# Kernel tuning notes

Measured on AMD Instinct MI355X. Metric: run time of the kernel, lower is better.

Reference implementation:

```python
import jax, jax.numpy as jnp
import numpy as np

N, E = 10000, 30000
D_IN, E_DIM, H1, H2, C = 64, 16, 128, 64, 10


def setup_inputs() -> dict:
    key = jax.random.key(0)
    ks = jax.random.split(key, 12)
    x = jax.random.normal(ks[0], (N, D_IN), dtype=jnp.float32)
    edge_attr = jax.random.normal(ks[1], (E, E_DIM), dtype=jnp.float32)
    edge_index = jax.random.randint(ks[2], (2, E), 0, N, dtype=jnp.int64)
    # linear1: D_IN -> H1
    W1 = jax.random.normal(ks[3], (D_IN, H1), dtype=jnp.float32) / np.sqrt(D_IN)
    b1 = jnp.zeros((H1,), dtype=jnp.float32)
    # edge MLP 1: E_DIM -> H1*H2
    We1 = jax.random.normal(ks[4], (E_DIM, H1 * H2), dtype=jnp.float32) / np.sqrt(E_DIM)
    be1 = jnp.zeros((H1 * H2,), dtype=jnp.float32)
    root1 = jax.random.uniform(ks[5], (H1, H2), dtype=jnp.float32,
                               minval=-1.0 / np.sqrt(H1), maxval=1.0 / np.sqrt(H1))
    bias1 = jnp.zeros((H2,), dtype=jnp.float32)
    # edge MLP 2: E_DIM -> H2*C
    We2 = jax.random.normal(ks[6], (E_DIM, H2 * C), dtype=jnp.float32) / np.sqrt(E_DIM)
    be2 = jnp.zeros((H2 * C,), dtype=jnp.float32)
    root2 = jax.random.uniform(ks[7], (H2, C), dtype=jnp.float32,
                               minval=-1.0 / np.sqrt(H2), maxval=1.0 / np.sqrt(H2))
    bias2 = jnp.zeros((C,), dtype=jnp.float32)
    return {"x": x, "edge_attr": edge_attr, "edge_index": edge_index,
            "W1": W1, "b1": b1, "We1": We1, "be1": be1, "root1": root1, "bias1": bias1,
            "We2": We2, "be2": be2, "root2": root2, "bias2": bias2}


def _nnconv(h, src, dst, edge_attr, We, be, root, bias, c_in, c_out):
    # per-edge weight matrix from edge MLP: [E, c_in, c_out]
    W_e = (edge_attr @ We + be).reshape(-1, c_in, c_out)
    msg = jnp.einsum('ei,eio->eo', h[src], W_e)          # gather + batched matmul
    agg = jax.ops.segment_sum(msg, dst, num_segments=N)   # scatter-add to target nodes
    return agg + h @ root + bias


def reference(x, edge_attr, edge_index, W1, b1, We1, be1, root1, bias1,
              We2, be2, root2, bias2):
    src, dst = edge_index[0], edge_index[1]  # PyG: x_j = x[src], aggregate at dst
    h = jax.nn.relu(x @ W1 + b1)                               # [N, H1]
    h = jax.nn.relu(_nnconv(h, src, dst, edge_attr, We1, be1, root1, bias1, H1, H2))
    z = _nnconv(h, src, dst, edge_attr, We2, be2, root2, bias2, H2, C)
    return jax.nn.log_softmax(z, axis=1)
```

## Files before the change

### kernel.cpp

```cpp
#include <hip/hip_runtime.h>

#define N_NODES 10000
#define N_EDGES 30000
#define DIN     64
#define EDIM    16
#define H1      128
#define H2      64
#define C_OUT   10

typedef __bf16 bfrag __attribute__((ext_vector_type(8)));
typedef float  f32x4 __attribute__((ext_vector_type(4)));

__device__ __forceinline__ ushort f2bf(float f) {
    union { float f; unsigned u; } x; x.f = f;
    unsigned r = x.u + 0x7fffu + ((x.u >> 16) & 1u);
    return (ushort)(r >> 16);
}
__device__ __forceinline__ float bf2f(ushort s) {
    union { unsigned u; float f; } x; x.u = ((unsigned)s) << 16;
    return x.f;
}

#define KA_B1   1250
#define KA_B2   (KA_B1 + 576)
#define KA_B3   (KA_B2 + 48)
#define KA_B4   (KA_B3 + 181)
__global__ __launch_bounds__(256) void kA_prep(
        const float* __restrict__ x, const float* __restrict__ W1,
        const float* __restrict__ b1,
        const float* __restrict__ We1, const float* __restrict__ root1,
        const float* __restrict__ be1,
        const float* __restrict__ We2, const float* __restrict__ be2,
        const float* __restrict__ root2,
        ushort* __restrict__ h_bf, ushort* __restrict__ B1t,
        ushort* __restrict__ B2t, float* __restrict__ aggz) {
    int t = threadIdx.x;
    int bx = blockIdx.x;
    if (bx < KA_B1) {
        __shared__ float w_lds[DIN * H1];
        __shared__ float b_lds[H1];
        __shared__ float x_lds[8][DIN];
        for (int idx = t; idx < DIN * H1 / 4; idx += 256)
            ((float4*)w_lds)[idx] = ((const float4*)W1)[idx];
        if (t < H1) b_lds[t] = b1[t];
        int n0 = bx * 8;
        if (t < 128) {
            int row = t >> 4, c4 = t & 15;
            int n = n0 + row;
            float4 v = make_float4(0.f, 0.f, 0.f, 0.f);
            if (n < N_NODES) v = ((const float4*)(x + (size_t)n * DIN))[c4];
            ((float4*)(x_lds[row]))[c4] = v;
        }
        __syncthreads();
        int nl = t >> 5;
        int o  = (t & 31) * 4;
        int n  = n0 + nl;
        float4 acc = *(const float4*)&b_lds[o];
        #pragma unroll 8
        for (int i = 0; i < DIN; ++i) {
            float xv = x_lds[nl][i];
            float4 w = *(const float4*)&w_lds[i * H1 + o];
            acc.x = fmaf(xv, w.x, acc.x);
            acc.y = fmaf(xv, w.y, acc.y);
            acc.z = fmaf(xv, w.z, acc.z);
            acc.w = fmaf(xv, w.w, acc.w);
        }
        if (n < N_NODES) {
            ushort4 s;
            s.x = f2bf(fmaxf(acc.x, 0.f));
            s.y = f2bf(fmaxf(acc.y, 0.f));
            s.z = f2bf(fmaxf(acc.z, 0.f));
            s.w = f2bf(fmaxf(acc.w, 0.f));
            *(ushort4*)&h_bf[(size_t)n * H1 + o] = s;
        }
    } else if (bx < KA_B2) {
        int idx = (bx - KA_B1) * 256 + t;
        int c = idx >> 7, i = idx & 127;
        float v;
        if (c < 1024)      v = We1[(size_t)(c >> 6) * (H1 * H2) + i * 64 + (c & 63)];
        else if (c < 1088) v = root1[i * 64 + (c - 1024)];
        else               v = be1[i * 64 + (c - 1088)];
        B1t[idx] = f2bf(v);
    } else if (bx < KA_B3) {
        int idx = (bx - KA_B2) * 256 + t;
        int c = idx >> 6, j = idx & 63;
        float v = 0.f;
        if (c < 160)      v = We2[(size_t)(c / 10) * 640 + j * 10 + (c % 10)];
        else if (c < 170) v = be2[j * 10 + (c - 160)];
        else if (c < 180) v = root2[j * 10 + (c - 170)];
        B2t[idx] = f2bf(v);
    } else {
        int zb = bx - KA_B3;
        for (int i = zb * 256 + t; i < 185000; i += 181 * 256)
            ((float4*)aggz)[i] = make_float4(0.f, 0.f, 0.f, 0.f);
    }
}

__global__ __launch_bounds__(256) void k3_mfma(
        const ushort* __restrict__ h_bf, const ushort* __restrict__ Bt,
        const float* __restrict__ bias1,
        ushort* __restrict__ G1, float* __restrict__ hrb1, float* __restrict__ hb1) {
    int t = threadIdx.x;
    int wave = t >> 6, lane = t & 63;
    int quad = lane >> 4, lrow = lane & 15;
    int y = blockIdx.y;
    int nbase = blockIdx.x * 128 + wave * 32;
    int ar0 = nbase + lrow;       if (ar0 > N_NODES - 1) ar0 = N_NODES - 1;
    int ar1 = nbase + 16 + lrow;  if (ar1 > N_NODES - 1) ar1 = N_NODES - 1;
    const ushort* bbase = Bt + (size_t)y * 64 * 128;
    f32x4 acc0[4] = {}, acc1[4] = {};
    #pragma unroll
    for (int kc = 0; kc < 128; kc += 32) {
        bfrag a0 = *reinterpret_cast<const bfrag*>(h_bf + (size_t)ar0 * 128 + kc + quad * 8);
        bfrag a1 = *reinterpret_cast<const bfrag*>(h_bf + (size_t)ar1 * 128 + kc + quad * 8);
        #pragma unroll
        for (int ct = 0; ct < 4; ++ct) {
            bfrag b = *reinterpret_cast<const bfrag*>(
                bbase + (size_t)(ct * 16 + lrow) * 128 + kc + quad * 8);
            acc0[ct] = __builtin_amdgcn_mfma_f32_16x16x32_bf16(a0, b, acc0[ct], 0, 0, 0);
            acc1[ct] = __builtin_amdgcn_mfma_f32_16x16x32_bf16(a1, b, acc1[ct], 0, 0, 0);
        }
    }
    #pragma unroll
    for (int half = 0; half < 2; ++half) {
        int rbase = nbase + half * 16 + quad * 4;
        #pragma unroll
        for (int ct = 0; ct < 4; ++ct) {
            int col = ct * 16 + lrow;
            f32x4 a = half ? acc1[ct] : acc0[ct];
            #pragma unroll
            for (int r = 0; r < 4; ++r) {
                int n = rbase + r;
                if (n >= N_NODES) continue;
                float v = a[r];
                if (y < 16) {
                    G1[(size_t)n * 1024 + y * 64 + col] = f2bf(v);
                } else if (y == 16) {
                    hrb1[(size_t)n * 64 + col] = v + bias1[col];
                } else {
                    hb1[(size_t)n * 64 + col] = v;
                }
            }
        }
    }
}

__global__ __launch_bounds__(256) void k4_edge1(
        const float* __restrict__ ea, const int* __restrict__ src_idx,
        const int* __restrict__ dst_idx, const ushort* __restrict__ G1,
        const float* __restrict__ hb1, float* __restrict__ agg1) {
    int t = threadIdx.x;
    int e = blockIdx.x * 4 + (t >> 6);
    int o = t & 63;
    int s = src_idx[e], d = dst_idx[e];
    float m = hb1[(size_t)s * 64 + o];
    const ushort* g = G1 + (size_t)s * 1024 + o;
    const float* a = ea + (size_t)e * 16;
    #pragma unroll
    for (int k = 0; k < 16; ++k) m = fmaf(a[k], bf2f(g[k * 64]), m);
    atomicAdd(&agg1[(size_t)d * 64 + o], m);
}

__global__ __launch_bounds__(256) void k56_mfma(
        const float* __restrict__ agg1, const float* __restrict__ hrb1,
        const ushort* __restrict__ B2t, const float* __restrict__ bias2,
        float* __restrict__ G2, float* __restrict__ hb2, float* __restrict__ hr2) {
    int t = threadIdx.x;
    int wave = t >> 6, lane = t & 63;
    int quad = lane >> 4, lrow = lane & 15;
    int y = blockIdx.y;
    int n0 = blockIdx.x * 64 + wave * 16;
    int arow = n0 + lrow; if (arow > N_NODES - 1) arow = N_NODES - 1;
    f32x4 acc[4] = {};
    #pragma unroll
    for (int kc = 0; kc < 64; kc += 32) {
        size_t off = (size_t)arow * 64 + kc + quad * 8;
        f32x4 p0 = *(const f32x4*)(agg1 + off);
        f32x4 p1 = *(const f32x4*)(agg1 + off + 4);
        f32x4 q0 = *(const f32x4*)(hrb1 + off);
        f32x4 q1 = *(const f32x4*)(hrb1 + off + 4);
        bfrag a;
        #pragma unroll
        for (int j = 0; j < 4; ++j) {
            a[j]     = (__bf16)fmaxf(p0[j] + q0[j], 0.f);
            a[j + 4] = (__bf16)fmaxf(p1[j] + q1[j], 0.f);
        }
        #pragma unroll
        for (int ct = 0; ct < 4; ++ct) {
            bfrag b = *reinterpret_cast<const bfrag*>(
                B2t + (size_t)(y * 64 + ct * 16 + lrow) * 64 + kc + quad * 8);
            acc[ct] = __builtin_amdgcn_mfma_f32_16x16x32_bf16(a, b, acc[ct], 0, 0, 0);
        }
    }
    #pragma unroll
    for (int ct = 0; ct < 4; ++ct) {
        int cg = y * 64 + ct * 16 + lrow;
        #pragma unroll
        for (int r = 0; r < 4; ++r) {
            int n = n0 + quad * 4 + r;
            if (n >= N_NODES) continue;
            float v = acc[ct][r];
            if (cg < 160)      G2[(size_t)n * 160 + cg] = v;
            else if (cg < 170) hb2[(size_t)n * 10 + (cg - 160)] = v;
            else if (cg < 180) hr2[(size_t)n * 10 + (cg - 170)] = v + bias2[cg - 170];
        }
    }
}

__global__ void k7_edge2(const float* __restrict__ ea, const int* __restrict__ src_idx,
                         const int* __restrict__ dst_idx, const float* __restrict__ G2,
                         const float* __restrict__ hb2, float* __restrict__ agg2) {
    int e = blockIdx.x * blockDim.x + threadIdx.x;
    if (e >= N_EDGES) return;
    int s = src_idx[e], d = dst_idx[e];
    float msg[10];
    #pragma unroll
    for (int c = 0; c < 10; ++c) msg[c] = hb2[(size_t)s * 10 + c];
    const float* a = ea + (size_t)e * 16;
    const float* g = G2 + (size_t)s * 160;
    #pragma unroll
    for (int k = 0; k < 16; ++k) {
        float av = a[k];
        #pragma unroll
        for (int c = 0; c < 10; ++c) msg[c] = fmaf(av, g[k * 10 + c], msg[c]);
    }
    #pragma unroll
    for (int c = 0; c < 10; ++c) atomicAdd(&agg2[(size_t)d * 10 + c], msg[c]);
}

__global__ void k8_logsoftmax(const float* __restrict__ agg2, const float* __restrict__ hr2,
                              float* __restrict__ out) {
    int n = blockIdx.x * blockDim.x + threadIdx.x;
    if (n >= N_NODES) return;
    float z[10]; float m = -1e30f;
    #pragma unroll
    for (int c = 0; c < 10; ++c) {
        z[c] = agg2[(size_t)n * 10 + c] + hr2[(size_t)n * 10 + c];
        m = fmaxf(m, z[c]);
    }
    float s = 0.f;
    #pragma unroll
    for (int c = 0; c < 10; ++c) s += expf(z[c] - m);
    float ls = logf(s);
    #pragma unroll
    for (int c = 0; c < 10; ++c) out[(size_t)n * 10 + c] = z[c] - m - ls;
}

extern "C" void kernel_launch(void* const* d_in, const int* in_sizes, int n_in,
                              void* d_out, int out_size, void* d_ws, size_t ws_size,
                              hipStream_t stream) {
    const float* x     = (const float*)d_in[0];
    const float* ea    = (const float*)d_in[1];
    const int*   eidx  = (const int*)d_in[2];
    const float* W1    = (const float*)d_in[3];
    const float* b1    = (const float*)d_in[4];
    const float* We1   = (const float*)d_in[5];
    const float* be1   = (const float*)d_in[6];
    const float* root1 = (const float*)d_in[7];
    const float* bias1 = (const float*)d_in[8];
    const float* We2   = (const float*)d_in[9];
    const float* be2   = (const float*)d_in[10];
    const float* root2 = (const float*)d_in[11];
    const float* bias2 = (const float*)d_in[12];
    float* out = (float*)d_out;

    float* ws = (float*)d_ws;
    ushort* h_bf = (ushort*)ws;
    ushort* B1t  = (ushort*)(ws + 640000);
    ushort* B2t  = (ushort*)(ws + 713728);
    ushort* G1   = (ushort*)(ws + 719872);
    float* hrb1 = ws + 719872 + 5120000;
    float* hb1  = hrb1 + 640000;
    float* agg1 = hb1  + 640000;
    float* agg2 = agg1 + 640000;
    float* G2   = agg2 + 100000;
    float* hb2  = G2   + 1600000;
    float* hr2  = hb2  + 100000;

    kA_prep<<<KA_B4, 256, 0, stream>>>(x, W1, b1, We1, root1, be1, We2, be2, root2,
                                       h_bf, B1t, B2t, agg1);
    k3_mfma<<<dim3(79, 18), 256, 0, stream>>>(h_bf, B1t, bias1, G1, hrb1, hb1);
    k4_edge1<<<7500, 256, 0, stream>>>(ea, eidx, eidx + N_EDGES, G1, hb1, agg1);
    k56_mfma<<<dim3(157, 3), 256, 0, stream>>>(agg1, hrb1, B2t, bias2, G2, hb2, hr2);
    k7_edge2<<<118, 256, 0, stream>>>(ea, eidx, eidx + N_EDGES, G2, hb2, agg2);
    k8_logsoftmax<<<40, 256, 0, stream>>>(agg2, hr2, out);
}
```

Baseline: 163.0 us.

## Fuse all six stages into one persistent kernel with software grid barriers

Replaces the six separate kernel launches with one persistent kernel of 512 blocks, in which each stage runs as a grid-stride loop over its original tiles and stages are separated by an atomic-counter grid barrier. The barrier counter is reset with a memset before each launch. The goal is to remove launch overhead and the idle gaps between the small dependent kernels. In exchange, each stage now runs on a fixed block count, the barriers spin, and correctness depends on all 512 blocks being resident at the same time (launch bounds allow 2 blocks per CU). Block-level parallelism in the large stages drops, for example the edge-1 stage goes from 7500 blocks to 512.

```diff
diff --git a/kernel.cpp b/kernel.cpp
--- a/kernel.cpp
+++ b/kernel.cpp
@@ -7,6 +7,7 @@
 #define H1      128
 #define H2      64
 #define C_OUT   10
+#define NB      512
 
 typedef __bf16 bfrag __attribute__((ext_vector_type(8)));
 typedef float  f32x4 __attribute__((ext_vector_type(4)));
@@ -21,35 +22,79 @@
     return x.f;
 }
 
-#define KA_B1   1250
-#define KA_B2   (KA_B1 + 576)
-#define KA_B3   (KA_B2 + 48)
-#define KA_B4   (KA_B3 + 181)
-__global__ __launch_bounds__(256) void kA_prep(
-        const float* __restrict__ x, const float* __restrict__ W1,
-        const float* __restrict__ b1,
+__device__ __forceinline__ void grid_sync(unsigned* bar, unsigned epoch) {
+    __syncthreads();
+    if (threadIdx.x == 0) {
+        __threadfence();
+        unsigned prev = atomicAdd(&bar[0], 1u);
+        if (prev == epoch * NB + (NB - 1)) {
+            __hip_atomic_store(&bar[1], epoch + 1, __ATOMIC_RELEASE,
+                               __HIP_MEMORY_SCOPE_AGENT);
+        } else {
+            while (__hip_atomic_load(&bar[1], __ATOMIC_ACQUIRE,
+                                     __HIP_MEMORY_SCOPE_AGENT) < epoch + 1) {
+                __builtin_amdgcn_s_sleep(16);
+            }
+        }
+        __threadfence();
+    }
+    __syncthreads();
+}
+
+__global__ __launch_bounds__(256, 2) void mega(
+        const float* __restrict__ x, const float* __restrict__ ea,
+        const int* __restrict__ src_idx, const int* __restrict__ dst_idx,
+        const float* __restrict__ W1, const float* __restrict__ b1,
         const float* __restrict__ We1, const float* __restrict__ root1,
-        const float* __restrict__ be1,
+        const float* __restrict__ be1, const float* __restrict__ bias1,
         const float* __restrict__ We2, const float* __restrict__ be2,
-        const float* __restrict__ root2,
+        const float* __restrict__ root2, const float* __restrict__ bias2,
         ushort* __restrict__ h_bf, ushort* __restrict__ B1t,
-        ushort* __restrict__ B2t, float* __restrict__ aggz) {
+        ushort* __restrict__ B2t, ushort* __restrict__ G1,
+        float* __restrict__ hrb1, float* __restrict__ hb1,
+        float* __restrict__ agg1, float* __restrict__ agg2,
+        float* __restrict__ G2, float* __restrict__ hb2, float* __restrict__ hr2,
+        float* __restrict__ out, unsigned* bar) {
+    __shared__ float smem[DIN * H1 + H1 + 8 * DIN];
+    float* w_lds = smem;
+    float* b_lds = smem + DIN * H1;
+    float* x_lds = smem + DIN * H1 + H1;
     int t = threadIdx.x;
     int bx = blockIdx.x;
-    if (bx < KA_B1) {
-        __shared__ float w_lds[DIN * H1];
-        __shared__ float b_lds[H1];
-        __shared__ float x_lds[8][DIN];
-        for (int idx = t; idx < DIN * H1 / 4; idx += 256)
-            ((float4*)w_lds)[idx] = ((const float4*)W1)[idx];
-        if (t < H1) b_lds[t] = b1[t];
-        int n0 = bx * 8;
+    int gtid = bx * 256 + t;
+    int wave = t >> 6, lane = t & 63;
+    int quad = lane >> 4, lrow = lane & 15;
+
+    for (int idx = gtid; idx < 1152 * 128; idx += NB * 256) {
+        int c = idx >> 7, i = idx & 127;
+        float v;
+        if (c < 1024)      v = We1[(size_t)(c >> 6) * (H1 * H2) + i * 64 + (c & 63)];
+        else if (c < 1088) v = root1[i * 64 + (c - 1024)];
+        else               v = be1[i * 64 + (c - 1088)];
+        B1t[idx] = f2bf(v);
+    }
+    for (int idx = gtid; idx < 192 * 64; idx += NB * 256) {
+        int c = idx >> 6, j = idx & 63;
+        float v = 0.f;
+        if (c < 160)      v = We2[(size_t)(c / 10) * 640 + j * 10 + (c % 10)];
+        else if (c < 170) v = be2[j * 10 + (c - 160)];
+        else if (c < 180) v = root2[j * 10 + (c - 170)];
+        B2t[idx] = f2bf(v);
+    }
+    for (int i = gtid; i < 185000; i += NB * 256)
+        ((float4*)agg1)[i] = make_float4(0.f, 0.f, 0.f, 0.f);
+    for (int idx = t; idx < DIN * H1 / 4; idx += 256)
+        ((float4*)w_lds)[idx] = ((const float4*)W1)[idx];
+    if (t < H1) b_lds[t] = b1[t];
+    for (int tile = bx; tile < 1250; tile += NB) {
+        __syncthreads();
+        int n0 = tile * 8;
         if (t < 128) {
             int row = t >> 4, c4 = t & 15;
             int n = n0 + row;
             float4 v = make_float4(0.f, 0.f, 0.f, 0.f);
             if (n < N_NODES) v = ((const float4*)(x + (size_t)n * DIN))[c4];
-            ((float4*)(x_lds[row]))[c4] = v;
+            ((float4*)(x_lds + row * DIN))[c4] = v;
         }
         __syncthreads();
         int nl = t >> 5;
@@ -58,7 +103,7 @@
         float4 acc = *(const float4*)&b_lds[o];
         #pragma unroll 8
         for (int i = 0; i < DIN; ++i) {
-            float xv = x_lds[nl][i];
+            float xv = x_lds[nl * DIN + i];
             float4 w = *(const float4*)&w_lds[i * H1 + o];
             acc.x = fmaf(xv, w.x, acc.x);
             acc.y = fmaf(xv, w.y, acc.y);
@@ -73,177 +118,140 @@
             s.w = f2bf(fmaxf(acc.w, 0.f));
             *(ushort4*)&h_bf[(size_t)n * H1 + o] = s;
         }
-    } else if (bx < KA_B2) {
-        int idx = (bx - KA_B1) * 256 + t;
-        int c = idx >> 7, i = idx & 127;
-        float v;
-        if (c < 1024)      v = We1[(size_t)(c >> 6) * (H1 * H2) + i * 64 + (c & 63)];
-        else if (c < 1088) v = root1[i * 64 + (c - 1024)];
-        else               v = be1[i * 64 + (c - 1088)];
-        B1t[idx] = f2bf(v);
-    } else if (bx < KA_B3) {
-        int idx = (bx - KA_B2) * 256 + t;
-        int c = idx >> 6, j = idx & 63;
-        float v = 0.f;
-        if (c < 160)      v = We2[(size_t)(c / 10) * 640 + j * 10 + (c % 10)];
-        else if (c < 170) v = be2[j * 10 + (c - 160)];
-        else if (c < 180) v = root2[j * 10 + (c - 170)];
-        B2t[idx] = f2bf(v);
-    } else {
-        int zb = bx - KA_B3;
-        for (int i = zb * 256 + t; i < 185000; i += 181 * 256)
-            ((float4*)aggz)[i] = make_float4(0.f, 0.f, 0.f, 0.f);
-    }
-}
-
-__global__ __launch_bounds__(256) void k3_mfma(
-        const ushort* __restrict__ h_bf, const ushort* __restrict__ Bt,
-        const float* __restrict__ bias1,
-        ushort* __restrict__ G1, float* __restrict__ hrb1, float* __restrict__ hb1) {
-    int t = threadIdx.x;
-    int wave = t >> 6, lane = t & 63;
-    int quad = lane >> 4, lrow = lane & 15;
-    int y = blockIdx.y;
-    int nbase = blockIdx.x * 128 + wave * 32;
-    int ar0 = nbase + lrow;       if (ar0 > N_NODES - 1) ar0 = N_NODES - 1;
-    int ar1 = nbase + 16 + lrow;  if (ar1 > N_NODES - 1) ar1 = N_NODES - 1;
-    const ushort* bbase = Bt + (size_t)y * 64 * 128;
-    f32x4 acc0[4] = {}, acc1[4] = {};
-    #pragma unroll
-    for (int kc = 0; kc < 128; kc += 32) {
-        bfrag a0 = *reinterpret_cast<const bfrag*>(h_bf + (size_t)ar0 * 128 + kc + quad * 8);
-        bfrag a1 = *reinterpret_cast<const bfrag*>(h_bf + (size_t)ar1 * 128 + kc + quad * 8);
+    }
+    grid_sync(bar, 0);
+
+    for (int tile = bx; tile < 79 * 18; tile += NB) {
+        int y = tile / 79;
+        int mx = tile - y * 79;
+        int nbase = mx * 128 + wave * 32;
+        int ar0 = nbase + lrow;       if (ar0 > N_NODES - 1) ar0 = N_NODES - 1;
+        int ar1 = nbase + 16 + lrow;  if (ar1 > N_NODES - 1) ar1 = N_NODES - 1;
+        const ushort* bbase = B1t + (size_t)y * 64 * 128;
+        f32x4 acc0[4] = {}, acc1[4] = {};
+        #pragma unroll
+        for (int kc = 0; kc < 128; kc += 32) {
+            bfrag a0 = *reinterpret_cast<const bfrag*>(h_bf + (size_t)ar0 * 128 + kc + quad * 8);
+            bfrag a1 = *reinterpret_cast<const bfrag*>(h_bf + (size_t)ar1 * 128 + kc + quad * 8);
+            #pragma unroll
+            for (int ct = 0; ct < 4; ++ct) {
+                bfrag b = *reinterpret_cast<const bfrag*>(
+                    bbase + (size_t)(ct * 16 + lrow) * 128 + kc + quad * 8);
+                acc0[ct] = __builtin_amdgcn_mfma_f32_16x16x32_bf16(a0, b, acc0[ct], 0, 0, 0);
+                acc1[ct] = __builtin_amdgcn_mfma_f32_16x16x32_bf16(a1, b, acc1[ct], 0, 0, 0);
+            }
+        }
+        #pragma unroll
+        for (int half = 0; half < 2; ++half) {
+            int rbase = nbase + half * 16 + quad * 4;
+            #pragma unroll
+            for (int ct = 0; ct < 4; ++ct) {
+                int col = ct * 16 + lrow;
+                f32x4 a = half ? acc1[ct] : acc0[ct];
+                #pragma unroll
+                for (int r = 0; r < 4; ++r) {
+                    int n = rbase + r;
+                    if (n >= N_NODES) continue;
+                    float v = a[r];
+                    if (y < 16) {
+                        G1[(size_t)n * 1024 + y * 64 + col] = f2bf(v);
+                    } else if (y == 16) {
+                        hrb1[(size_t)n * 64 + col] = v + bias1[col];
+                    } else {
+                        hb1[(size_t)n * 64 + col] = v;
+                    }
+                }
+            }
+        }
+    }
+    grid_sync(bar, 1);
+
+    for (int e = bx * 4 + wave; e < N_EDGES; e += NB * 4) {
+        int s = src_idx[e], d = dst_idx[e];
+        int o = lane;
+        float m = hb1[(size_t)s * 64 + o];
+        const ushort* g = G1 + (size_t)s * 1024 + o;
+        const float* a = ea + (size_t)e * 16;
+        #pragma unroll
+        for (int k = 0; k < 16; ++k) m = fmaf(a[k], bf2f(g[k * 64]), m);
+        atomicAdd(&agg1[(size_t)d * 64 + o], m);
+    }
+    grid_sync(bar, 2);
+
+    for (int tile = bx; tile < 157 * 3; tile += NB) {
+        int y = tile / 157;
+        int mx = tile - y * 157;
+        int n0 = mx * 64 + wave * 16;
+        int arow = n0 + lrow; if (arow > N_NODES - 1) arow = N_NODES - 1;
+        f32x4 acc[4] = {};
+        #pragma unroll
+        for (int kc = 0; kc < 64; kc += 32) {
+            size_t off = (size_t)arow * 64 + kc + quad * 8;
+            f32x4 p0 = *(const f32x4*)(agg1 + off);
+            f32x4 p1 = *(const f32x4*)(agg1 + off + 4);
+            f32x4 q0 = *(const f32x4*)(hrb1 + off);
+            f32x4 q1 = *(const f32x4*)(hrb1 + off + 4);
+            bfrag a;
+            #pragma unroll
+            for (int j = 0; j < 4; ++j) {
+                a[j]     = (__bf16)fmaxf(p0[j] + q0[j], 0.f);
+                a[j + 4] = (__bf16)fmaxf(p1[j] + q1[j], 0.f);
+            }
+            #pragma unroll
+            for (int ct = 0; ct < 4; ++ct) {
+                bfrag b = *reinterpret_cast<const bfrag*>(
+                    B2t + (size_t)(y * 64 + ct * 16 + lrow) * 64 + kc + quad * 8);
+                acc[ct] = __builtin_amdgcn_mfma_f32_16x16x32_bf16(a, b, acc[ct], 0, 0, 0);
+            }
+        }
         #pragma unroll
         for (int ct = 0; ct < 4; ++ct) {
-            bfrag b = *reinterpret_cast<const bfrag*>(
-                bbase + (size_t)(ct * 16 + lrow) * 128 + kc + quad * 8);
-            acc0[ct] = __builtin_amdgcn_mfma_f32_16x16x32_bf16(a0, b, acc0[ct], 0, 0, 0);
-            acc1[ct] = __builtin_amdgcn_mfma_f32_16x16x32_bf16(a1, b, acc1[ct], 0, 0, 0);
-        }
-    }
-    #pragma unroll
-    for (int half = 0; half < 2; ++half) {
-        int rbase = nbase + half * 16 + quad * 4;
-        #pragma unroll
-        for (int ct = 0; ct < 4; ++ct) {
-            int col = ct * 16 + lrow;
-            f32x4 a = half ? acc1[ct] : acc0[ct];
+            int cg = y * 64 + ct * 16 + lrow;
             #pragma unroll
             for (int r = 0; r < 4; ++r) {
-                int n = rbase + r;
+                int n = n0 + quad * 4 + r;
                 if (n >= N_NODES) continue;
-                float v = a[r];
-                if (y < 16) {
-                    G1[(size_t)n * 1024 + y * 64 + col] = f2bf(v);
-                } else if (y == 16) {
-                    hrb1[(size_t)n * 64 + col] = v + bias1[col];
-                } else {
-                    hb1[(size_t)n * 64 + col] = v;
-                }
-            }
-        }
-    }
-}
-
-__global__ __launch_bounds__(256) void k4_edge1(
-        const float* __restrict__ ea, const int* __restrict__ src_idx,
-        const int* __restrict__ dst_idx, const ushort* __restrict__ G1,
-        const float* __restrict__ hb1, float* __restrict__ agg1) {
-    int t = threadIdx.x;
-    int e = blockIdx.x * 4 + (t >> 6);
-    int o = t & 63;
-    int s = src_idx[e], d = dst_idx[e];
-    float m = hb1[(size_t)s * 64 + o];
-    const ushort* g = G1 + (size_t)s * 1024 + o;
-    const float* a = ea + (size_t)e * 16;
-    #pragma unroll
-    for (int k = 0; k < 16; ++k) m = fmaf(a[k], bf2f(g[k * 64]), m);
-    atomicAdd(&agg1[(size_t)d * 64 + o], m);
-}
-
-__global__ __launch_bounds__(256) void k56_mfma(
-        const float* __restrict__ agg1, const float* __restrict__ hrb1,
-        const ushort* __restrict__ B2t, const float* __restrict__ bias2,
-        float* __restrict__ G2, float* __restrict__ hb2, float* __restrict__ hr2) {
-    int t = threadIdx.x;
-    int wave = t >> 6, lane = t & 63;
-    int quad = lane >> 4, lrow = lane & 15;
-    int y = blockIdx.y;
-    int n0 = blockIdx.x * 64 + wave * 16;
-    int arow = n0 + lrow; if (arow > N_NODES - 1) arow = N_NODES - 1;
-    f32x4 acc[4] = {};
-    #pragma unroll
-    for (int kc = 0; kc < 64; kc += 32) {
-        size_t off = (size_t)arow * 64 + kc + quad * 8;
-        f32x4 p0 = *(const f32x4*)(agg1 + off);
-        f32x4 p1 = *(const f32x4*)(agg1 + off + 4);
-        f32x4 q0 = *(const f32x4*)(hrb1 + off);
-        f32x4 q1 = *(const f32x4*)(hrb1 + off + 4);
-        bfrag a;
-        #pragma unroll
-        for (int j = 0; j < 4; ++j) {
-            a[j]     = (__bf16)fmaxf(p0[j] + q0[j], 0.f);
-            a[j + 4] = (__bf16)fmaxf(p1[j] + q1[j], 0.f);
-        }
-        #pragma unroll
-        for (int ct = 0; ct < 4; ++ct) {
-            bfrag b = *reinterpret_cast<const bfrag*>(
-                B2t + (size_t)(y * 64 + ct * 16 + lrow) * 64 + kc + quad * 8);
-            acc[ct] = __builtin_amdgcn_mfma_f32_16x16x32_bf16(a, b, acc[ct], 0, 0, 0);
-        }
-    }
-    #pragma unroll
-    for (int ct = 0; ct < 4; ++ct) {
-        int cg = y * 64 + ct * 16 + lrow;
-        #pragma unroll
-        for (int r = 0; r < 4; ++r) {
-            int n = n0 + quad * 4 + r;
-            if (n >= N_NODES) continue;
-            float v = acc[ct][r];
-            if (cg < 160)      G2[(size_t)n * 160 + cg] = v;
-            else if (cg < 170) hb2[(size_t)n * 10 + (cg - 160)] = v;
-            else if (cg < 180) hr2[(size_t)n * 10 + (cg - 170)] = v + bias2[cg - 170];
-        }
-    }
-}
-
-__global__ void k7_edge2(const float* __restrict__ ea, const int* __restrict__ src_idx,
-                         const int* __restrict__ dst_idx, const float* __restrict__ G2,
-                         const float* __restrict__ hb2, float* __restrict__ agg2) {
-    int e = blockIdx.x * blockDim.x + threadIdx.x;
-    if (e >= N_EDGES) return;
-    int s = src_idx[e], d = dst_idx[e];
-    float msg[10];
-    #pragma unroll
-    for (int c = 0; c < 10; ++c) msg[c] = hb2[(size_t)s * 10 + c];
-    const float* a = ea + (size_t)e * 16;
-    const float* g = G2 + (size_t)s * 160;
-    #pragma unroll
-    for (int k = 0; k < 16; ++k) {
-        float av = a[k];
-        #pragma unroll
-        for (int c = 0; c < 10; ++c) msg[c] = fmaf(av, g[k * 10 + c], msg[c]);
-    }
-    #pragma unroll
-    for (int c = 0; c < 10; ++c) atomicAdd(&agg2[(size_t)d * 10 + c], msg[c]);
-}
-
-__global__ void k8_logsoftmax(const float* __restrict__ agg2, const float* __restrict__ hr2,
-                              float* __restrict__ out) {
-    int n = blockIdx.x * blockDim.x + threadIdx.x;
-    if (n >= N_NODES) return;
-    float z[10]; float m = -1e30f;
-    #pragma unroll
-    for (int c = 0; c < 10; ++c) {
-        z[c] = agg2[(size_t)n * 10 + c] + hr2[(size_t)n * 10 + c];
-        m = fmaxf(m, z[c]);
-    }
-    float s = 0.f;
-    #pragma unroll
-    for (int c = 0; c < 10; ++c) s += expf(z[c] - m);
-    float ls = logf(s);
-    #pragma unroll
-    for (int c = 0; c < 10; ++c) out[(size_t)n * 10 + c] = z[c] - m - ls;
+                float v = acc[ct][r];
+                if (cg < 160)      G2[(size_t)n * 160 + cg] = v;
+                else if (cg < 170) hb2[(size_t)n * 10 + (cg - 160)] = v;
+                else if (cg < 180) hr2[(size_t)n * 10 + (cg - 170)] = v + bias2[cg - 170];
+            }
+        }
+    }
+    grid_sync(bar, 3);
+
+    for (int e = gtid; e < N_EDGES; e += NB * 256) {
+        int s = src_idx[e], d = dst_idx[e];
+        float msg[10];
+        #pragma unroll
+        for (int c = 0; c < 10; ++c) msg[c] = hb2[(size_t)s * 10 + c];
+        const float* a = ea + (size_t)e * 16;
+        const float* g = G2 + (size_t)s * 160;
+        #pragma unroll
+        for (int k = 0; k < 16; ++k) {
+            float av = a[k];
+            #pragma unroll
+            for (int c = 0; c < 10; ++c) msg[c] = fmaf(av, g[k * 10 + c], msg[c]);
+        }
+        #pragma unroll
+        for (int c = 0; c < 10; ++c) atomicAdd(&agg2[(size_t)d * 10 + c], msg[c]);
+    }
+    grid_sync(bar, 4);
+
+    for (int n = gtid; n < N_NODES; n += NB * 256) {
+        float z[10]; float m = -1e30f;
+        #pragma unroll
+        for (int c = 0; c < 10; ++c) {
+            z[c] = agg2[(size_t)n * 10 + c] + hr2[(size_t)n * 10 + c];
+            m = fmaxf(m, z[c]);
+        }
+        float s = 0.f;
+        #pragma unroll
+        for (int c = 0; c < 10; ++c) s += expf(z[c] - m);
+        float ls = logf(s);
+        #pragma unroll
+        for (int c = 0; c < 10; ++c) out[(size_t)n * 10 + c] = z[c] - m - ls;
+    }
 }
 
 extern "C" void kernel_launch(void* const* d_in, const int* in_sizes, int n_in,
@@ -276,12 +284,12 @@
     float* G2   = agg2 + 100000;
     float* hb2  = G2   + 1600000;
     float* hr2  = hb2  + 100000;
-
-    kA_prep<<<KA_B4, 256, 0, stream>>>(x, W1, b1, We1, root1, be1, We2, be2, root2,
-                                       h_bf, B1t, B2t, agg1);
-    k3_mfma<<<dim3(79, 18), 256, 0, stream>>>(h_bf, B1t, bias1, G1, hrb1, hb1);
-    k4_edge1<<<7500, 256, 0, stream>>>(ea, eidx, eidx + N_EDGES, G1, hb1, agg1);
-    k56_mfma<<<dim3(157, 3), 256, 0, stream>>>(agg1, hrb1, B2t, bias2, G2, hb2, hr2);
-    k7_edge2<<<118, 256, 0, stream>>>(ea, eidx, eidx + N_EDGES, G2, hb2, agg2);
-    k8_logsoftmax<<<40, 256, 0, stream>>>(agg2, hr2, out);
-}
+    unsigned* bar = (unsigned*)(hr2 + 100000);
+
+    hipMemsetAsync(bar, 0, 2 * sizeof(unsigned), stream);
+    mega<<<NB, 256, 0, stream>>>(x, ea, eidx, eidx + N_EDGES,
+                                 W1, b1, We1, root1, be1, bias1,
+                                 We2, be2, root2, bias2,
+                                 h_bf, B1t, B2t, G1, hrb1, hb1,
+                                 agg1, agg2, G2, hb2, hr2, out, bar);
+}
```

New measurement: 553.3 us. 3.39x slower.

## Transpose per-node edge-weight tables so edge kernels load contiguous vectors

Applied to the files above, without the earlier changes.

The G1 and G2 intermediate tables are now written k-minor (output channel major), so each lane of the edge kernels reads its 16 k-values as contiguous vector loads instead of 16 strided scalar loads. The second edge kernel is also reparallelised from one thread per edge (10 outputs and 10 atomics each) to one thread per (edge, class), giving ten times as many threads. In exchange, the MFMA epilogue stores become scattered with a 16-element stride, and each lane in the first edge kernel now reads 32 bytes at a 32-byte stride, which may coalesce less well than the previous layout where adjacent lanes read adjacent elements.

```diff
diff --git a/kernel.cpp b/kernel.cpp
--- a/kernel.cpp
+++ b/kernel.cpp
@@ -10,6 +10,7 @@
 
 typedef __bf16 bfrag __attribute__((ext_vector_type(8)));
 typedef float  f32x4 __attribute__((ext_vector_type(4)));
+typedef ushort ushort8 __attribute__((ext_vector_type(8)));
 
 __device__ __forceinline__ ushort f2bf(float f) {
     union { float f; unsigned u; } x; x.f = f;
@@ -99,7 +100,7 @@
 __global__ __launch_bounds__(256) void k3_mfma(
         const ushort* __restrict__ h_bf, const ushort* __restrict__ Bt,
         const float* __restrict__ bias1,
-        ushort* __restrict__ G1, float* __restrict__ hrb1, float* __restrict__ hb1) {
+        ushort* __restrict__ G1t, float* __restrict__ hrb1, float* __restrict__ hb1) {
     int t = threadIdx.x;
     int wave = t >> 6, lane = t & 63;
     int quad = lane >> 4, lrow = lane & 15;
@@ -134,7 +135,7 @@
                 if (n >= N_NODES) continue;
                 float v = a[r];
                 if (y < 16) {
-                    G1[(size_t)n * 1024 + y * 64 + col] = f2bf(v);
+                    G1t[(size_t)n * 1024 + col * 16 + y] = f2bf(v);
                 } else if (y == 16) {
                     hrb1[(size_t)n * 64 + col] = v + bias1[col];
                 } else {
@@ -147,24 +148,28 @@
 
 __global__ __launch_bounds__(256) void k4_edge1(
         const float* __restrict__ ea, const int* __restrict__ src_idx,
-        const int* __restrict__ dst_idx, const ushort* __restrict__ G1,
+        const int* __restrict__ dst_idx, const ushort* __restrict__ G1t,
         const float* __restrict__ hb1, float* __restrict__ agg1) {
     int t = threadIdx.x;
     int e = blockIdx.x * 4 + (t >> 6);
     int o = t & 63;
     int s = src_idx[e], d = dst_idx[e];
     float m = hb1[(size_t)s * 64 + o];
-    const ushort* g = G1 + (size_t)s * 1024 + o;
+    const ushort* g = G1t + (size_t)s * 1024 + o * 16;
+    ushort8 g0 = *reinterpret_cast<const ushort8*>(g);
+    ushort8 g1 = *reinterpret_cast<const ushort8*>(g + 8);
     const float* a = ea + (size_t)e * 16;
     #pragma unroll
-    for (int k = 0; k < 16; ++k) m = fmaf(a[k], bf2f(g[k * 64]), m);
+    for (int k = 0; k < 8; ++k) m = fmaf(a[k], bf2f(g0[k]), m);
+    #pragma unroll
+    for (int k = 0; k < 8; ++k) m = fmaf(a[k + 8], bf2f(g1[k]), m);
     atomicAdd(&agg1[(size_t)d * 64 + o], m);
 }
 
 __global__ __launch_bounds__(256) void k56_mfma(
         const float* __restrict__ agg1, const float* __restrict__ hrb1,
         const ushort* __restrict__ B2t, const float* __restrict__ bias2,
-        float* __restrict__ G2, float* __restrict__ hb2, float* __restrict__ hr2) {
+        float* __restrict__ G2t, float* __restrict__ hb2, float* __restrict__ hr2) {
     int t = threadIdx.x;
     int wave = t >> 6, lane = t & 63;
     int quad = lane >> 4, lrow = lane & 15;
@@ -195,37 +200,42 @@
     #pragma unroll
     for (int ct = 0; ct < 4; ++ct) {
         int cg = y * 64 + ct * 16 + lrow;
+        int kk = cg / 10, cc = cg - kk * 10;
         #pragma unroll
         for (int r = 0; r < 4; ++r) {
             int n = n0 + quad * 4 + r;
             if (n >= N_NODES) continue;
             float v = acc[ct][r];
-            if (cg < 160)      G2[(size_t)n * 160 + cg] = v;
+            if (cg < 160)      G2t[(size_t)n * 160 + cc * 16 + kk] = v;
             else if (cg < 170) hb2[(size_t)n * 10 + (cg - 160)] = v;
             else if (cg < 180) hr2[(size_t)n * 10 + (cg - 170)] = v + bias2[cg - 170];
         }
     }
 }
 
-__global__ void k7_edge2(const float* __restrict__ ea, const int* __restrict__ src_idx,
-                         const int* __restrict__ dst_idx, const float* __restrict__ G2,
-                         const float* __restrict__ hb2, float* __restrict__ agg2) {
-    int e = blockIdx.x * blockDim.x + threadIdx.x;
-    if (e >= N_EDGES) return;
+__global__ __launch_bounds__(256) void k7_edge2(
+        const float* __restrict__ ea, const int* __restrict__ src_idx,
+        const int* __restrict__ dst_idx, const float* __restrict__ G2t,
+        const float* __restrict__ hb2, float* __restrict__ agg2) {
+    int tid = blockIdx.x * 256 + threadIdx.x;
+    if (tid >= N_EDGES * 10) return;
+    int e = tid / 10, c = tid - e * 10;
     int s = src_idx[e], d = dst_idx[e];
-    float msg[10];
-    #pragma unroll
-    for (int c = 0; c < 10; ++c) msg[c] = hb2[(size_t)s * 10 + c];
+    float m = hb2[(size_t)s * 10 + c];
+    const float* g = G2t + (size_t)s * 160 + c * 16;
     const float* a = ea + (size_t)e * 16;
-    const float* g = G2 + (size_t)s * 160;
-    #pragma unroll
-    for (int k = 0; k < 16; ++k) {
-        float av = a[k];
-        #pragma unroll
-        for (int c = 0; c < 10; ++c) msg[c] = fmaf(av, g[k * 10 + c], msg[c]);
-    }
-    #pragma unroll
-    for (int c = 0; c < 10; ++c) atomicAdd(&agg2[(size_t)d * 10 + c], msg[c]);
+    f32x4 g0 = *(const f32x4*)g,       g1 = *(const f32x4*)(g + 4);
+    f32x4 g2 = *(const f32x4*)(g + 8), g3 = *(const f32x4*)(g + 12);
+    f32x4 a0 = *(const f32x4*)a,       a1 = *(const f32x4*)(a + 4);
+    f32x4 a2 = *(const f32x4*)(a + 8), a3 = *(const f32x4*)(a + 12);
+    #pragma unroll
+    for (int k = 0; k < 4; ++k) {
+        m = fmaf(a0[k], g0[k], m);
+        m = fmaf(a1[k], g1[k], m);
+        m = fmaf(a2[k], g2[k], m);
+        m = fmaf(a3[k], g3[k], m);
+    }
+    atomicAdd(&agg2[(size_t)d * 10 + c], m);
 }
 
 __global__ void k8_logsoftmax(const float* __restrict__ agg2, const float* __restrict__ hr2,
@@ -268,20 +278,20 @@
     ushort* h_bf = (ushort*)ws;
     ushort* B1t  = (ushort*)(ws + 640000);
     ushort* B2t  = (ushort*)(ws + 713728);
-    ushort* G1   = (ushort*)(ws + 719872);
+    ushort* G1t  = (ushort*)(ws + 719872);
     float* hrb1 = ws + 719872 + 5120000;
     float* hb1  = hrb1 + 640000;
     float* agg1 = hb1  + 640000;
     float* agg2 = agg1 + 640000;
-    float* G2   = agg2 + 100000;
-    float* hb2  = G2   + 1600000;
+    float* G2t  = agg2 + 100000;
+    float* hb2  = G2t  + 1600000;
     float* hr2  = hb2  + 100000;
 
     kA_prep<<<KA_B4, 256, 0, stream>>>(x, W1, b1, We1, root1, be1, We2, be2, root2,
                                        h_bf, B1t, B2t, agg1);
-    k3_mfma<<<dim3(79, 18), 256, 0, stream>>>(h_bf, B1t, bias1, G1, hrb1, hb1);
-    k4_edge1<<<7500, 256, 0, stream>>>(ea, eidx, eidx + N_EDGES, G1, hb1, agg1);
-    k56_mfma<<<dim3(157, 3), 256, 0, stream>>>(agg1, hrb1, B2t, bias2, G2, hb2, hr2);
-    k7_edge2<<<118, 256, 0, stream>>>(ea, eidx, eidx + N_EDGES, G2, hb2, agg2);
+    k3_mfma<<<dim3(79, 18), 256, 0, stream>>>(h_bf, B1t, bias1, G1t, hrb1, hb1);
+    k4_edge1<<<7500, 256, 0, stream>>>(ea, eidx, eidx + N_EDGES, G1t, hb1, agg1);
+    k56_mfma<<<dim3(157, 3), 256, 0, stream>>>(agg1, hrb1, B2t, bias2, G2t, hb2, hr2);
+    k7_edge2<<<1172, 256, 0, stream>>>(ea, eidx, eidx + N_EDGES, G2t, hb2, agg2);
     k8_logsoftmax<<<40, 256, 0, stream>>>(agg2, hr2, out);
 }
```

Result: slower. 201.7 us (+23.8%).
